# Kernel optimization log

Measured on AMD Instinct MI355X. Metric: run time of the kernel, lower is better.

The kernel has to match this reference:

```python
import jax, jax.numpy as jnp
import numpy as np

NUM_EXPERTS = 32
TOP_K = 4
HIDDEN = 2048
INTER = 768


def setup_inputs() -> dict:
    key = jax.random.key(0)
    k1, k2, k3, k4 = jax.random.split(key, 4)
    hidden_states = jax.random.normal(k1, (4, 512, HIDDEN), dtype=jnp.float32)
    gate = jax.random.normal(k2, (HIDDEN, NUM_EXPERTS), dtype=jnp.float32) * 0.02
    gate_up_proj = jax.random.normal(k3, (NUM_EXPERTS, HIDDEN, 2 * INTER), dtype=jnp.float32) * 0.02
    down_proj = jax.random.normal(k4, (NUM_EXPERTS, INTER, HIDDEN), dtype=jnp.float32) * 0.02
    return {"hidden_states": hidden_states, "gate": gate,
            "gate_up_proj": gate_up_proj, "down_proj": down_proj}


def reference(hidden_states, gate, gate_up_proj, down_proj):
    batch_size = hidden_states.shape[0]
    x = hidden_states.reshape(-1, HIDDEN)  # (T, D)
    num_tokens = x.shape[0]

    # Router
    router_logits = jnp.einsum('TD,DE->TE', x, gate)
    routing_weights = jax.nn.softmax(router_logits.astype(jnp.float32), axis=-1)
    top_k_weights, top_k_indices = jax.lax.top_k(routing_weights, TOP_K)
    top_k_weights = top_k_weights / top_k_weights.sum(axis=-1, keepdims=True)
    top_k_weights = top_k_weights.astype(x.dtype)

    # Scatter top-k weights into full (T, E) matrix
    router_weights = jnp.zeros((num_tokens, NUM_EXPERTS), dtype=x.dtype)
    token_indices = jnp.broadcast_to(jnp.arange(num_tokens)[:, None], top_k_indices.shape)
    router_weights = router_weights.at[token_indices, top_k_indices].set(top_k_weights)

    # Dense all-expert experts pass (faithful to original: computes every expert per token)
    gate_up = jnp.einsum('TD,EDF->TEF', x, gate_up_proj)  # (T, E, 2F)
    g, u = jnp.split(gate_up, 2, axis=-1)
    gated = u * jax.nn.silu(g)  # (T, E, F)
    next_states = jnp.einsum('TEF,EFD->TED', gated, down_proj)
    next_states = (next_states * router_weights[..., None]).sum(axis=1)  # (T, D)
    return next_states.reshape(batch_size, -1, HIDDEN)
```

## Files before the change

### kernel.cpp

```cpp
#include <hip/hip_runtime.h>

#define T_TOKENS 2048
#define HIDDEN   2048
#define NEXPERT  32
#define TOPK     4
#define INTER    768
#define NPAIRS   (T_TOKENS*TOPK)
#define BM       128
#define BK       32
#define MT_MAX   95
#define NT1      24
#define NT2      32
#define NK1      (HIDDEN/BK)
#define NK2      (INTER/BK)

typedef short  bh8 __attribute__((ext_vector_type(8)));
typedef float  fx4 __attribute__((ext_vector_type(4)));

#define AS1 __attribute__((address_space(1)))
#define AS3 __attribute__((address_space(3)))

__device__ __forceinline__ void gload_lds16(const void* g, const void* lds_generic){
    __builtin_amdgcn_global_load_lds(
        (const AS1 void*)(unsigned long long)g,
        (AS3 void*)(unsigned int)(unsigned long long)lds_generic,
        16, 0, 0);
}

__device__ __forceinline__ unsigned int pack2bf(float a, float b){
    unsigned ua = __float_as_uint(a) + 0x8000u;
    unsigned ub = __float_as_uint(b) + 0x8000u;
    return __builtin_amdgcn_perm(ub, ua, 0x07060302u);
}
__device__ __forceinline__ unsigned short f2bfu(float f){
    return (unsigned short)((__float_as_uint(f) + 0x8000u) >> 16);
}

__global__ void cvt_x_k(const float* __restrict__ x, unsigned short* __restrict__ xb){
    int i = (blockIdx.x*256 + threadIdx.x)*8;
    float4 a = *(const float4*)(x+i);
    float4 b = *(const float4*)(x+i+4);
    uint4 o;
    o.x = pack2bf(a.x,a.y); o.y = pack2bf(a.z,a.w);
    o.z = pack2bf(b.x,b.y); o.w = pack2bf(b.z,b.w);
    *(uint4*)(xb+i) = o;
}

__global__ void router_k(const float* __restrict__ x, const float* __restrict__ gate,
                         int* __restrict__ topk_id, float* __restrict__ topk_w,
                         int* __restrict__ counts){
    const int t = blockIdx.x;
    const int l = threadIdx.x;
    const float* xr = x + (size_t)t*HIDDEN;
    float acc[NEXPERT];
#pragma unroll
    for (int e=0;e<NEXPERT;e++) acc[e]=0.f;
    for (int d=l; d<HIDDEN; d+=64){
        float xv = xr[d];
        const float4* g4 = (const float4*)(gate + (size_t)d*NEXPERT);
#pragma unroll
        for (int i=0;i<8;i++){
            float4 g = g4[i];
            acc[i*4+0] += xv*g.x; acc[i*4+1] += xv*g.y;
            acc[i*4+2] += xv*g.z; acc[i*4+3] += xv*g.w;
        }
    }
#pragma unroll
    for (int e=0;e<NEXPERT;e++){
#pragma unroll
        for (int m=1;m<64;m<<=1) acc[e] += __shfl_xor(acc[e], m, 64);
    }
    int ids[TOPK]; float lv[TOPK];
#pragma unroll
    for (int k=0;k<TOPK;k++){
        float m=-1e30f; int mi=0;
#pragma unroll
        for (int e=0;e<NEXPERT;e++){ if (acc[e]>m){ m=acc[e]; mi=e; } }
        ids[k]=mi; lv[k]=m; acc[mi]=-1e30f;
    }
    float ex[TOPK]; float s=0.f;
#pragma unroll
    for (int k=0;k<TOPK;k++){ ex[k]=__expf(lv[k]-lv[0]); s+=ex[k]; }
    if (l==0){
        float inv = 1.f/s;
#pragma unroll
        for (int k=0;k<TOPK;k++){
            topk_id[t*TOPK+k]=ids[k];
            topk_w[t*TOPK+k]=ex[k]*inv;
            atomicAdd(&counts[ids[k]],1);
        }
    }
}

__global__ void sched_k(const int* __restrict__ counts, int* __restrict__ offs,
                        int* __restrict__ cursors, int* __restrict__ nmt,
                        int* __restrict__ te, int* __restrict__ tr0, int* __restrict__ trn){
    if (threadIdx.x==0 && blockIdx.x==0){
        int tot=0, nm=0;
        for (int e=0;e<NEXPERT;e++){
            int c = counts[e];
            offs[e]=tot; cursors[e]=tot;
            for (int s=0;s<c;s+=BM){
                te[nm]=e; tr0[nm]=tot+s; trn[nm]=(c-s)<BM?(c-s):BM; nm++;
            }
            tot+=c;
        }
        *nmt = nm;
    }
}

__global__ void scatter_k(const int* __restrict__ topk_id, const float* __restrict__ topk_w,
                          int* __restrict__ cursors, int* __restrict__ pair_tok,
                          float* __restrict__ pair_w){
    int g = blockIdx.x*256 + threadIdx.x;
    int e = topk_id[g];
    float w = topk_w[g];
    int pos = atomicAdd(&cursors[e],1);
    pair_tok[pos] = g>>2;
    pair_w[pos]  = w;
}

#define TILE_DECODE(NT)                                            \
    const int nwg = gridDim.x;                                     \
    const int q = nwg>>3, r = nwg&7;                               \
    const int xcd = blockIdx.x & 7, bidx = blockIdx.x >> 3;        \
    const int L = (xcd<r ? xcd*(q+1) : r*(q+1)+(xcd-r)*q) + bidx;  \
    const int mt = L % MT_MAX, nt = L / MT_MAX;                    \
    if (mt >= *nmt) return;                                        \
    const int e = te[mt], row0 = tr0[mt], rows = trn[mt];

#define GSTEP(KK, NK, BSTR, C0, C1, C2, RL0, RL1, RW0, RW1) do{                 \
    int _ks = (KK)+2; if (_ks > (NK)-1) _ks = (NK)-1;                           \
    const float* _bp = bsrc + (size_t)_ks*BK*(BSTR);                            \
    RL0 = *(const float4*)(_bp);                                                \
    RL1 = *(const float4*)(_bp + (BSTR));                                       \
    gload_lds16(asrc0 + _ks*BK, &As[C2][(w*16)*32]);                            \
    gload_lds16(asrc1 + _ks*BK, &As[C2][(64+w*16)*32]);                         \
    {   const unsigned short* _Ak = As[C0];                                     \
        const char* _Bk = (const char*)Bs[C0];                                  \
        bh8 _a0 = *(const bh8*)(_Ak + (w*32+l15)*32    + ((kb^sA)<<3));         \
        bh8 _a1 = *(const bh8*)(_Ak + (w*32+16+l15)*32 + ((kb^sA)<<3));         \
        _Pragma("unroll")                                                       \
        for (int c=0;c<4;c++){                                                  \
            const int bc = c*16 + l15;                                          \
            bh8 _b = *(const bh8*)(_Bk + bc*80 + ((kb ^ ((bc>>3)&3))<<4));      \
            acc[0][c] = __builtin_amdgcn_mfma_f32_16x16x32_bf16(_a0,_b,acc[0][c],0,0,0); \
            acc[1][c] = __builtin_amdgcn_mfma_f32_16x16x32_bf16(_a1,_b,acc[1][c],0,0,0); \
        }                                                                       \
    }                                                                           \
    asm volatile("s_waitcnt vmcnt(4)" ::: "memory");                            \
    {   char* _bw = (char*)Bs[C1];                                              \
        *(unsigned*)(_bw + wb      ) = pack2bf(RW0.x, RW1.x);                   \
        *(unsigned*)(_bw + wb +  80) = pack2bf(RW0.y, RW1.y);                   \
        *(unsigned*)(_bw + wb + 160) = pack2bf(RW0.z, RW1.z);                   \
        *(unsigned*)(_bw + wb + 240) = pack2bf(RW0.w, RW1.w);                   \
    }                                                                           \
    asm volatile("s_waitcnt lgkmcnt(0)" ::: "memory");                          \
    __builtin_amdgcn_s_barrier();                                               \
}while(0)

__global__ __launch_bounds__(256) void gemm1_k(
        const unsigned short* __restrict__ xb, const float* __restrict__ gup,
        const int* __restrict__ nmt, const int* __restrict__ te,
        const int* __restrict__ tr0, const int* __restrict__ trn,
        const int* __restrict__ pair_tok, const float* __restrict__ pair_w,
        unsigned short* __restrict__ gated){
    __shared__ __align__(16) unsigned short As[3][BM*32];
    __shared__ __align__(16) unsigned short Bs[3][64*40];
    __shared__ int   s_tok[BM];
    __shared__ float s_w[BM];

    TILE_DECODE(NT1)
    const int n0 = nt*32;

    const int t = threadIdx.x;
    if (t < BM){
        int p = row0 + t; if (p > NPAIRS-1) p = NPAIRS-1;
        s_tok[t] = pair_tok[p];
        s_w[t]   = pair_w[p];
    }
    __syncthreads();

    const int w = t>>6, lane = t&63;
    const int l15 = lane & 15, kb = lane >> 4;
    const int sA = (l15>>1)&3;

    const int arow0 = w*16 + (lane>>2);
    const int arow1 = 64 + arow0;
    const int ck0 = (lane&3) ^ ((lane>>3)&3);
    const unsigned short* asrc0 = xb + (size_t)s_tok[arow0]*HIDDEN + ck0*8;
    const unsigned short* asrc1 = xb + (size_t)s_tok[arow1]*HIDDEN + ck0*8;

    const int col4 = (t&15)*4;
    const int bd0  = (t>>4)*2;
    const int sB   = (col4>>3)&3;
    const unsigned wb = (unsigned)(col4*80 + (((bd0>>3) ^ sB)<<4) + (bd0&7)*2);
    const int fc = (col4 < 32) ? (n0 + col4) : (736 + n0 + col4);
    const float* bsrc = gup + (size_t)e*HIDDEN*(2*INTER) + (size_t)bd0*(2*INTER) + fc;

    fx4 acc[2][4];
#pragma unroll
    for (int i=0;i<2;i++)
#pragma unroll
        for (int j=0;j<4;j++) acc[i][j] = (fx4)0.f;

    float4 rE0, rE1, rO0, rO1;
    gload_lds16(asrc0,      &As[0][(w*16)*32]);
    gload_lds16(asrc1,      &As[0][(64+w*16)*32]);
    gload_lds16(asrc0 + BK, &As[1][(w*16)*32]);
    gload_lds16(asrc1 + BK, &As[1][(64+w*16)*32]);
    rE0 = *(const float4*)(bsrc);
    rE1 = *(const float4*)(bsrc + 2*INTER);
    rO0 = *(const float4*)(bsrc + (size_t)BK*2*INTER);
    rO1 = *(const float4*)(bsrc + (size_t)BK*2*INTER + 2*INTER);
    asm volatile("s_waitcnt vmcnt(0)" ::: "memory");
    {
        char* bw0 = (char*)Bs[0];
        *(unsigned*)(bw0 + wb      ) = pack2bf(rE0.x, rE1.x);
        *(unsigned*)(bw0 + wb +  80) = pack2bf(rE0.y, rE1.y);
        *(unsigned*)(bw0 + wb + 160) = pack2bf(rE0.z, rE1.z);
        *(unsigned*)(bw0 + wb + 240) = pack2bf(rE0.w, rE1.w);
    }
    asm volatile("s_waitcnt lgkmcnt(0)" ::: "memory");
    __builtin_amdgcn_s_barrier();

    int c0 = 0;
    for (int k2 = 0; k2 < NK1; k2 += 2){
        int c1 = c0+1; if (c1==3) c1 = 0;
        int c2 = c1+1; if (c2==3) c2 = 0;
        GSTEP(k2,   NK1, 2*INTER, c0, c1, c2, rE0, rE1, rO0, rO1);
        GSTEP(k2+1, NK1, 2*INTER, c1, c2, c0, rO0, rO1, rE0, rE1);
        c0 = c2;
    }
    asm volatile("s_waitcnt vmcnt(0)" ::: "memory");

    const int rbase = w*32 + kb*4;
#pragma unroll
    for (int mr=0;mr<2;mr++){
#pragma unroll
        for (int qq=0;qq<4;qq++){
            int row = rbase + mr*16 + qq;
            if (row < rows){
                float wgt = s_w[row];
                size_t prow = (size_t)(row0 + row)*INTER + n0 + l15;
#pragma unroll
                for (int c=0;c<2;c++){
                    float g = acc[mr][c][qq], u = acc[mr][c+2][qq];
                    float sil = g / (1.f + __expf(-g));
                    gated[prow + c*16] = f2bfu(sil*u*wgt);
                }
            }
        }
    }
}

__global__ __launch_bounds__(256) void gemm2_k(
        const unsigned short* __restrict__ gated, const float* __restrict__ down,
        const int* __restrict__ nmt, const int* __restrict__ te,
        const int* __restrict__ tr0, const int* __restrict__ trn,
        const int* __restrict__ pair_tok, float* __restrict__ out){
    __shared__ __align__(16) unsigned short As[3][BM*32];
    __shared__ __align__(16) unsigned short Bs[3][64*40];
    __shared__ int s_tok[BM];

    TILE_DECODE(NT2)
    const int n0 = nt*64;

    const int t = threadIdx.x;
    if (t < BM){
        int p = row0 + t; if (p > NPAIRS-1) p = NPAIRS-1;
        s_tok[t] = pair_tok[p];
    }
    __syncthreads();

    const int w = t>>6, lane = t&63;
    const int l15 = lane & 15, kb = lane >> 4;
    const int sA = (l15>>1)&3;

    const int arow0 = w*16 + (lane>>2);
    const int arow1 = 64 + arow0;
    const int ck0 = (lane&3) ^ ((lane>>3)&3);
    int ap0 = row0 + arow0; if (ap0 > NPAIRS-1) ap0 = NPAIRS-1;
    int ap1 = row0 + arow1; if (ap1 > NPAIRS-1) ap1 = NPAIRS-1;
    const unsigned short* asrc0 = gated + (size_t)ap0*INTER + ck0*8;
    const unsigned short* asrc1 = gated + (size_t)ap1*INTER + ck0*8;

    const int col4 = (t&15)*4;
    const int bd0  = (t>>4)*2;
    const int sB   = (col4>>3)&3;
    const unsigned wb = (unsigned)(col4*80 + (((bd0>>3) ^ sB)<<4) + (bd0&7)*2);
    const float* bsrc = down + (size_t)e*INTER*HIDDEN + (size_t)bd0*HIDDEN + (n0 + col4);

    fx4 acc[2][4];
#pragma unroll
    for (int i=0;i<2;i++)
#pragma unroll
        for (int j=0;j<4;j++) acc[i][j] = (fx4)0.f;

    float4 rE0, rE1, rO0, rO1;
    gload_lds16(asrc0,      &As[0][(w*16)*32]);
    gload_lds16(asrc1,      &As[0][(64+w*16)*32]);
    gload_lds16(asrc0 + BK, &As[1][(w*16)*32]);
    gload_lds16(asrc1 + BK, &As[1][(64+w*16)*32]);
    rE0 = *(const float4*)(bsrc);
    rE1 = *(const float4*)(bsrc + HIDDEN);
    rO0 = *(const float4*)(bsrc + (size_t)BK*HIDDEN);
    rO1 = *(const float4*)(bsrc + (size_t)BK*HIDDEN + HIDDEN);
    asm volatile("s_waitcnt vmcnt(0)" ::: "memory");
    {
        char* bw0 = (char*)Bs[0];
        *(unsigned*)(bw0 + wb      ) = pack2bf(rE0.x, rE1.x);
        *(unsigned*)(bw0 + wb +  80) = pack2bf(rE0.y, rE1.y);
        *(unsigned*)(bw0 + wb + 160) = pack2bf(rE0.z, rE1.z);
        *(unsigned*)(bw0 + wb + 240) = pack2bf(rE0.w, rE1.w);
    }
    asm volatile("s_waitcnt lgkmcnt(0)" ::: "memory");
    __builtin_amdgcn_s_barrier();

    int c0 = 0;
    for (int k2 = 0; k2 < NK2; k2 += 2){
        int c1 = c0+1; if (c1==3) c1 = 0;
        int c2 = c1+1; if (c2==3) c2 = 0;
        GSTEP(k2,   NK2, HIDDEN, c0, c1, c2, rE0, rE1, rO0, rO1);
        GSTEP(k2+1, NK2, HIDDEN, c1, c2, c0, rO0, rO1, rE0, rE1);
        c0 = c2;
    }
    asm volatile("s_waitcnt vmcnt(0)" ::: "memory");

    const int rbase = w*32 + kb*4;
#pragma unroll
    for (int mr=0;mr<2;mr++){
#pragma unroll
        for (int qq=0;qq<4;qq++){
            int row = rbase + mr*16 + qq;
            if (row < rows){
                float* orow = out + (size_t)s_tok[row]*HIDDEN + n0 + l15;
#pragma unroll
                for (int c=0;c<4;c++)
                    atomicAdd(orow + c*16, acc[mr][c][qq]);
            }
        }
    }
}

extern "C" void kernel_launch(void* const* d_in, const int* in_sizes, int n_in,
                              void* d_out, int out_size, void* d_ws, size_t ws_size,
                              hipStream_t stream){
    const float* x    = (const float*)d_in[0];
    const float* gate = (const float*)d_in[1];
    const float* gup  = (const float*)d_in[2];
    const float* down = (const float*)d_in[3];
    float* out = (float*)d_out;
    char*  ws  = (char*)d_ws;

    int*   topk_id  = (int*)  (ws + 0x00000);
    float* topk_w   = (float*)(ws + 0x08000);
    int*   counts   = (int*)  (ws + 0x10000);
    int*   cursors  = (int*)  (ws + 0x10080);
    int*   offs     = (int*)  (ws + 0x10100);
    int*   nmt      = (int*)  (ws + 0x10180);
    int*   te       = (int*)  (ws + 0x10200);
    int*   tr0      = (int*)  (ws + 0x10400);
    int*   trn      = (int*)  (ws + 0x10600);
    int*   pair_tok = (int*)  (ws + 0x10800);
    float* pair_w   = (float*)(ws + 0x18800);
    unsigned short* gated = (unsigned short*)(ws + 0x21000);
    unsigned short* xb    = (unsigned short*)(ws + 0xC60000);

    hipMemsetAsync(d_out, 0, (size_t)out_size*sizeof(float), stream);
    hipMemsetAsync(counts, 0, NEXPERT*sizeof(int), stream);

    cvt_x_k  <<<T_TOKENS*HIDDEN/(256*8), 256, 0, stream>>>(x, xb);
    router_k <<<T_TOKENS, 64, 0, stream>>>(x, gate, topk_id, topk_w, counts);
    sched_k  <<<1, 64, 0, stream>>>(counts, offs, cursors, nmt, te, tr0, trn);
    scatter_k<<<NPAIRS/256, 256, 0, stream>>>(topk_id, topk_w, cursors, pair_tok, pair_w);
    gemm1_k  <<<MT_MAX*NT1, 256, 0, stream>>>(xb, gup, nmt, te, tr0, trn, pair_tok, pair_w, gated);
    gemm2_k  <<<MT_MAX*NT2, 256, 0, stream>>>(gated, down, nmt, te, tr0, trn, pair_tok, out);
}
```

Baseline: 477.2 us.

## Double N-tile width and deepen global prefetch pipeline in both expert GEMMs

Both grouped GEMM kernels now compute 128-wide B tiles (64 gate plus 64 up columns in gemm1, 128 output columns in gemm2), which halves the number of N tiles so each A tile loaded from LDS is reused across twice as many MFMAs. The B prefetch moves to three register stages, three k-steps ahead, with four A LDS buffers and two B LDS buffers. This cuts redundant A traffic and the number of workgroups, at the cost of more accumulators and prefetch registers per thread and fewer blocks to fill the GPU.

After: 448.2 us. -6.1%, faster.

```diff
diff --git a/kernel.cpp b/kernel.cpp
--- a/kernel.cpp
+++ b/kernel.cpp
@@ -9,8 +9,8 @@
 #define BM       128
 #define BK       32
 #define MT_MAX   95
-#define NT1      24
-#define NT2      32
+#define NT1      12
+#define NT2      16
 #define NK1      (HIDDEN/BK)
 #define NK2      (INTER/BK)
 
@@ -129,34 +129,53 @@
     if (mt >= *nmt) return;                                        \
     const int e = te[mt], row0 = tr0[mt], rows = trn[mt];
 
-#define GSTEP(KK, NK, BSTR, C0, C1, C2, RL0, RL1, RW0, RW1) do{                 \
-    int _ks = (KK)+2; if (_ks > (NK)-1) _ks = (NK)-1;                           \
+#define PSTEP(KK, NK, BSTR, I0,I1,I2,I3, W0,W1,W2,W3) do{                       \
+    int _ks = (KK)+3; if (_ks > (NK)-1) _ks = (NK)-1;                           \
     const float* _bp = bsrc + (size_t)_ks*BK*(BSTR);                            \
-    RL0 = *(const float4*)(_bp);                                                \
-    RL1 = *(const float4*)(_bp + (BSTR));                                       \
-    gload_lds16(asrc0 + _ks*BK, &As[C2][(w*16)*32]);                            \
-    gload_lds16(asrc1 + _ks*BK, &As[C2][(64+w*16)*32]);                         \
-    {   const unsigned short* _Ak = As[C0];                                     \
-        const char* _Bk = (const char*)Bs[C0];                                  \
+    I0 = *(const float4*)(_bp);                                                 \
+    I1 = *(const float4*)(_bp + (BSTR));                                        \
+    I2 = *(const float4*)(_bp + 2*(BSTR));                                      \
+    I3 = *(const float4*)(_bp + 3*(BSTR));                                      \
+    gload_lds16(asrc0 + _ks*BK, &As[aW][(w*16)*32]);                            \
+    gload_lds16(asrc1 + _ks*BK, &As[aW][(64+w*16)*32]);                         \
+    {   const unsigned short* _Ak = As[aR];                                     \
+        const char* _Bk = (const char*)Bs[bRd];                                 \
         bh8 _a0 = *(const bh8*)(_Ak + (w*32+l15)*32    + ((kb^sA)<<3));         \
         bh8 _a1 = *(const bh8*)(_Ak + (w*32+16+l15)*32 + ((kb^sA)<<3));         \
         _Pragma("unroll")                                                       \
-        for (int c=0;c<4;c++){                                                  \
+        for (int c=0;c<8;c++){                                                  \
             const int bc = c*16 + l15;                                          \
             bh8 _b = *(const bh8*)(_Bk + bc*80 + ((kb ^ ((bc>>3)&3))<<4));      \
             acc[0][c] = __builtin_amdgcn_mfma_f32_16x16x32_bf16(_a0,_b,acc[0][c],0,0,0); \
             acc[1][c] = __builtin_amdgcn_mfma_f32_16x16x32_bf16(_a1,_b,acc[1][c],0,0,0); \
         }                                                                       \
     }                                                                           \
-    asm volatile("s_waitcnt vmcnt(4)" ::: "memory");                            \
-    {   char* _bw = (char*)Bs[C1];                                              \
-        *(unsigned*)(_bw + wb      ) = pack2bf(RW0.x, RW1.x);                   \
-        *(unsigned*)(_bw + wb +  80) = pack2bf(RW0.y, RW1.y);                   \
-        *(unsigned*)(_bw + wb + 160) = pack2bf(RW0.z, RW1.z);                   \
-        *(unsigned*)(_bw + wb + 240) = pack2bf(RW0.w, RW1.w);                   \
+    asm volatile("s_waitcnt vmcnt(12)" ::: "memory");                           \
+    {   char* _bw = (char*)Bs[bRd^1];                                           \
+        *(uint2*)(_bw + wb      ) = make_uint2(pack2bf(W0.x,W1.x), pack2bf(W2.x,W3.x)); \
+        *(uint2*)(_bw + wb +  80) = make_uint2(pack2bf(W0.y,W1.y), pack2bf(W2.y,W3.y)); \
+        *(uint2*)(_bw + wb + 160) = make_uint2(pack2bf(W0.z,W1.z), pack2bf(W2.z,W3.z)); \
+        *(uint2*)(_bw + wb + 240) = make_uint2(pack2bf(W0.w,W1.w), pack2bf(W2.w,W3.w)); \
     }                                                                           \
     asm volatile("s_waitcnt lgkmcnt(0)" ::: "memory");                          \
     __builtin_amdgcn_s_barrier();                                               \
+    aR=(aR+1)&3; aW=(aW+1)&3; bRd^=1;                                           \
+}while(0)
+
+#define LDB(SET0,SET1,SET2,SET3, KS, BSTR) do{                                  \
+    const float* _bp = bsrc + (size_t)(KS)*BK*(BSTR);                           \
+    SET0 = *(const float4*)(_bp);                                               \
+    SET1 = *(const float4*)(_bp + (BSTR));                                      \
+    SET2 = *(const float4*)(_bp + 2*(BSTR));                                    \
+    SET3 = *(const float4*)(_bp + 3*(BSTR));                                    \
+}while(0)
+
+#define WRB0(W0,W1,W2,W3) do{                                                   \
+    char* _bw = (char*)Bs[0];                                                   \
+    *(uint2*)(_bw + wb      ) = make_uint2(pack2bf(W0.x,W1.x), pack2bf(W2.x,W3.x)); \
+    *(uint2*)(_bw + wb +  80) = make_uint2(pack2bf(W0.y,W1.y), pack2bf(W2.y,W3.y)); \
+    *(uint2*)(_bw + wb + 160) = make_uint2(pack2bf(W0.z,W1.z), pack2bf(W2.z,W3.z)); \
+    *(uint2*)(_bw + wb + 240) = make_uint2(pack2bf(W0.w,W1.w), pack2bf(W2.w,W3.w)); \
 }while(0)
 
 __global__ __launch_bounds__(256) void gemm1_k(
@@ -165,13 +184,13 @@
         const int* __restrict__ tr0, const int* __restrict__ trn,
         const int* __restrict__ pair_tok, const float* __restrict__ pair_w,
         unsigned short* __restrict__ gated){
-    __shared__ __align__(16) unsigned short As[3][BM*32];
-    __shared__ __align__(16) unsigned short Bs[3][64*40];
+    __shared__ __align__(16) unsigned short As[4][BM*32];
+    __shared__ __align__(16) unsigned short Bs[2][128*40];
     __shared__ int   s_tok[BM];
     __shared__ float s_w[BM];
 
     TILE_DECODE(NT1)
-    const int n0 = nt*32;
+    const int n0 = nt*64;
 
     const int t = threadIdx.x;
     if (t < BM){
@@ -191,47 +210,42 @@
     const unsigned short* asrc0 = xb + (size_t)s_tok[arow0]*HIDDEN + ck0*8;
     const unsigned short* asrc1 = xb + (size_t)s_tok[arow1]*HIDDEN + ck0*8;
 
-    const int col4 = (t&15)*4;
-    const int bd0  = (t>>4)*2;
-    const int sB   = (col4>>3)&3;
-    const unsigned wb = (unsigned)(col4*80 + (((bd0>>3) ^ sB)<<4) + (bd0&7)*2);
-    const int fc = (col4 < 32) ? (n0 + col4) : (736 + n0 + col4);
+    const int j5 = t & 31, col4 = j5*4;
+    const int bd0  = (t>>5)*4;
+    const int gq = (j5>>1)&3;
+    const unsigned wb = (unsigned)(col4*80 + (((bd0>>3) ^ gq)<<4) + (bd0&4)*2);
+    const int fc = (col4 < 64) ? (n0 + col4) : (704 + n0 + col4);
     const float* bsrc = gup + (size_t)e*HIDDEN*(2*INTER) + (size_t)bd0*(2*INTER) + fc;
 
-    fx4 acc[2][4];
+    fx4 acc[2][8];
 #pragma unroll
     for (int i=0;i<2;i++)
 #pragma unroll
-        for (int j=0;j<4;j++) acc[i][j] = (fx4)0.f;
-
-    float4 rE0, rE1, rO0, rO1;
-    gload_lds16(asrc0,      &As[0][(w*16)*32]);
-    gload_lds16(asrc1,      &As[0][(64+w*16)*32]);
-    gload_lds16(asrc0 + BK, &As[1][(w*16)*32]);
-    gload_lds16(asrc1 + BK, &As[1][(64+w*16)*32]);
-    rE0 = *(const float4*)(bsrc);
-    rE1 = *(const float4*)(bsrc + 2*INTER);
-    rO0 = *(const float4*)(bsrc + (size_t)BK*2*INTER);
-    rO1 = *(const float4*)(bsrc + (size_t)BK*2*INTER + 2*INTER);
-    asm volatile("s_waitcnt vmcnt(0)" ::: "memory");
-    {
-        char* bw0 = (char*)Bs[0];
-        *(unsigned*)(bw0 + wb      ) = pack2bf(rE0.x, rE1.x);
-        *(unsigned*)(bw0 + wb +  80) = pack2bf(rE0.y, rE1.y);
-        *(unsigned*)(bw0 + wb + 160) = pack2bf(rE0.z, rE1.z);
-        *(unsigned*)(bw0 + wb + 240) = pack2bf(rE0.w, rE1.w);
-    }
+        for (int j=0;j<8;j++) acc[i][j] = (fx4)0.f;
+
+    float4 s0_0,s0_1,s0_2,s0_3, s1_0,s1_1,s1_2,s1_3, s2_0,s2_1,s2_2,s2_3;
+
+    LDB(s0_0,s0_1,s0_2,s0_3, 0, 2*INTER);
+    gload_lds16(asrc0,        &As[0][(w*16)*32]);
+    gload_lds16(asrc1,        &As[0][(64+w*16)*32]);
+    LDB(s1_0,s1_1,s1_2,s1_3, 1, 2*INTER);
+    gload_lds16(asrc0 + BK,   &As[1][(w*16)*32]);
+    gload_lds16(asrc1 + BK,   &As[1][(64+w*16)*32]);
+    LDB(s2_0,s2_1,s2_2,s2_3, 2, 2*INTER);
+    gload_lds16(asrc0 + 2*BK, &As[2][(w*16)*32]);
+    gload_lds16(asrc1 + 2*BK, &As[2][(64+w*16)*32]);
+    asm volatile("s_waitcnt vmcnt(12)" ::: "memory");
+    WRB0(s0_0,s0_1,s0_2,s0_3);
     asm volatile("s_waitcnt lgkmcnt(0)" ::: "memory");
     __builtin_amdgcn_s_barrier();
 
-    int c0 = 0;
-    for (int k2 = 0; k2 < NK1; k2 += 2){
-        int c1 = c0+1; if (c1==3) c1 = 0;
-        int c2 = c1+1; if (c2==3) c2 = 0;
-        GSTEP(k2,   NK1, 2*INTER, c0, c1, c2, rE0, rE1, rO0, rO1);
-        GSTEP(k2+1, NK1, 2*INTER, c1, c2, c0, rO0, rO1, rE0, rE1);
-        c0 = c2;
-    }
+    int aR=0, aW=3, bRd=0;
+    for (int k3=0; k3<NK1-1; k3+=3){
+        PSTEP(k3,   NK1, 2*INTER, s0_0,s0_1,s0_2,s0_3, s1_0,s1_1,s1_2,s1_3);
+        PSTEP(k3+1, NK1, 2*INTER, s1_0,s1_1,s1_2,s1_3, s2_0,s2_1,s2_2,s2_3);
+        PSTEP(k3+2, NK1, 2*INTER, s2_0,s2_1,s2_2,s2_3, s0_0,s0_1,s0_2,s0_3);
+    }
+    PSTEP(NK1-1, NK1, 2*INTER, s0_0,s0_1,s0_2,s0_3, s1_0,s1_1,s1_2,s1_3);
     asm volatile("s_waitcnt vmcnt(0)" ::: "memory");
 
     const int rbase = w*32 + kb*4;
@@ -244,8 +258,8 @@
                 float wgt = s_w[row];
                 size_t prow = (size_t)(row0 + row)*INTER + n0 + l15;
 #pragma unroll
-                for (int c=0;c<2;c++){
-                    float g = acc[mr][c][qq], u = acc[mr][c+2][qq];
+                for (int c=0;c<4;c++){
+                    float g = acc[mr][c][qq], u = acc[mr][c+4][qq];
                     float sil = g / (1.f + __expf(-g));
                     gated[prow + c*16] = f2bfu(sil*u*wgt);
                 }
@@ -259,12 +273,12 @@
         const int* __restrict__ nmt, const int* __restrict__ te,
         const int* __restrict__ tr0, const int* __restrict__ trn,
         const int* __restrict__ pair_tok, float* __restrict__ out){
-    __shared__ __align__(16) unsigned short As[3][BM*32];
-    __shared__ __align__(16) unsigned short Bs[3][64*40];
+    __shared__ __align__(16) unsigned short As[4][BM*32];
+    __shared__ __align__(16) unsigned short Bs[2][128*40];
     __shared__ int s_tok[BM];
 
     TILE_DECODE(NT2)
-    const int n0 = nt*64;
+    const int n0 = nt*128;
 
     const int t = threadIdx.x;
     if (t < BM){
@@ -285,45 +299,39 @@
     const unsigned short* asrc0 = gated + (size_t)ap0*INTER + ck0*8;
     const unsigned short* asrc1 = gated + (size_t)ap1*INTER + ck0*8;
 
-    const int col4 = (t&15)*4;
-    const int bd0  = (t>>4)*2;
-    const int sB   = (col4>>3)&3;
-    const unsigned wb = (unsigned)(col4*80 + (((bd0>>3) ^ sB)<<4) + (bd0&7)*2);
+    const int j5 = t & 31, col4 = j5*4;
+    const int bd0  = (t>>5)*4;
+    const int gq = (j5>>1)&3;
+    const unsigned wb = (unsigned)(col4*80 + (((bd0>>3) ^ gq)<<4) + (bd0&4)*2);
     const float* bsrc = down + (size_t)e*INTER*HIDDEN + (size_t)bd0*HIDDEN + (n0 + col4);
 
-    fx4 acc[2][4];
+    fx4 acc[2][8];
 #pragma unroll
     for (int i=0;i<2;i++)
 #pragma unroll
-        for (int j=0;j<4;j++) acc[i][j] = (fx4)0.f;
-
-    float4 rE0, rE1, rO0, rO1;
-    gload_lds16(asrc0,      &As[0][(w*16)*32]);
-    gload_lds16(asrc1,      &As[0][(64+w*16)*32]);
-    gload_lds16(asrc0 + BK, &As[1][(w*16)*32]);
-    gload_lds16(asrc1 + BK, &As[1][(64+w*16)*32]);
-    rE0 = *(const float4*)(bsrc);
-    rE1 = *(const float4*)(bsrc + HIDDEN);
-    rO0 = *(const float4*)(bsrc + (size_t)BK*HIDDEN);
-    rO1 = *(const float4*)(bsrc + (size_t)BK*HIDDEN + HIDDEN);
-    asm volatile("s_waitcnt vmcnt(0)" ::: "memory");
-    {
-        char* bw0 = (char*)Bs[0];
-        *(unsigned*)(bw0 + wb      ) = pack2bf(rE0.x, rE1.x);
-        *(unsigned*)(bw0 + wb +  80) = pack2bf(rE0.y, rE1.y);
-        *(unsigned*)(bw0 + wb + 160) = pack2bf(rE0.z, rE1.z);
-        *(unsigned*)(bw0 + wb + 240) = pack2bf(rE0.w, rE1.w);
-    }
+        for (int j=0;j<8;j++) acc[i][j] = (fx4)0.f;
+
+    float4 s0_0,s0_1,s0_2,s0_3, s1_0,s1_1,s1_2,s1_3, s2_0,s2_1,s2_2,s2_3;
+
+    LDB(s0_0,s0_1,s0_2,s0_3, 0, HIDDEN);
+    gload_lds16(asrc0,        &As[0][(w*16)*32]);
+    gload_lds16(asrc1,        &As[0][(64+w*16)*32]);
+    LDB(s1_0,s1_1,s1_2,s1_3, 1, HIDDEN);
+    gload_lds16(asrc0 + BK,   &As[1][(w*16)*32]);
+    gload_lds16(asrc1 + BK,   &As[1][(64+w*16)*32]);
+    LDB(s2_0,s2_1,s2_2,s2_3, 2, HIDDEN);
+    gload_lds16(asrc0 + 2*BK, &As[2][(w*16)*32]);
+    gload_lds16(asrc1 + 2*BK, &As[2][(64+w*16)*32]);
+    asm volatile("s_waitcnt vmcnt(12)" ::: "memory");
+    WRB0(s0_0,s0_1,s0_2,s0_3);
     asm volatile("s_waitcnt lgkmcnt(0)" ::: "memory");
     __builtin_amdgcn_s_barrier();
 
-    int c0 = 0;
-    for (int k2 = 0; k2 < NK2; k2 += 2){
-        int c1 = c0+1; if (c1==3) c1 = 0;
-        int c2 = c1+1; if (c2==3) c2 = 0;
-        GSTEP(k2,   NK2, HIDDEN, c0, c1, c2, rE0, rE1, rO0, rO1);
-        GSTEP(k2+1, NK2, HIDDEN, c1, c2, c0, rO0, rO1, rE0, rE1);
-        c0 = c2;
+    int aR=0, aW=3, bRd=0;
+    for (int k3=0; k3<NK2; k3+=3){
+        PSTEP(k3,   NK2, HIDDEN, s0_0,s0_1,s0_2,s0_3, s1_0,s1_1,s1_2,s1_3);
+        PSTEP(k3+1, NK2, HIDDEN, s1_0,s1_1,s1_2,s1_3, s2_0,s2_1,s2_2,s2_3);
+        PSTEP(k3+2, NK2, HIDDEN, s2_0,s2_1,s2_2,s2_3, s0_0,s0_1,s0_2,s0_3);
     }
     asm volatile("s_waitcnt vmcnt(0)" ::: "memory");
 
@@ -336,7 +344,7 @@
             if (row < rows){
                 float* orow = out + (size_t)s_tok[row]*HIDDEN + n0 + l15;
 #pragma unroll
-                for (int c=0;c<4;c++)
+                for (int c=0;c<8;c++)
                     atomicAdd(orow + c*16, acc[mr][c][qq]);
             }
         }
```
